# Performance work log

Measured on AMD Instinct MI355X. Metric: run time of the kernel, lower is better.

The kernel has to match this reference:

```python
import jax, jax.numpy as jnp
import numpy as np

D = 20       # bond_dim (= virtual_dim = per-module output_dim)
BATCH = 128
BN_EPS = 1e-5


def _unfold(t, h, w, n):
    # torch x.unfold(2,h,h).unfold(3,w,w).reshape(b, C, -1, n)
    B, C, H, W = t.shape
    t = t.reshape(B, C, H // h, h, W // w, w).transpose(0, 1, 2, 4, 3, 5)
    return t.reshape(B, C, -1, n)


def _mps(x, cores, label):
    # x: [b, C, P, n] site values; cores: [P, n, D, F, D] with F = 2*C; label: [P, D, O, D]
    feat = jnp.concatenate([x, 1.0 - x], axis=1)              # [b, F, P, n]  ([x, 1-x] feature map)
    M = jnp.einsum('bfpn,pnufv->npbuv', feat, cores)           # [n, P, b, D, D] site matrices
    v = jnp.full((cores.shape[2],), cores.shape[2] ** -0.5, dtype=x.dtype)  # boundary vector
    left = jnp.einsum('u,pbuv->pbv', v, M[0])
    for i in range(1, M.shape[0]):                             # n is small & static (4 or 16)
        left = jnp.einsum('pbu,pbuv->pbv', left, M[i])
    return jnp.einsum('pbu,puov,v->bpo', left, label, v)       # [b, P, O]


def _bn(y, gamma, beta):
    # training-mode BatchNorm1d over channel axis 1 of [b, C, L]
    mean = y.mean(axis=(0, 2), keepdims=True)
    var = y.var(axis=(0, 2), keepdims=True)
    return (y - mean) * jax.lax.rsqrt(var + BN_EPS) * gamma[None, :, None] + beta[None, :, None]


def setup_inputs() -> dict:
    key = jax.random.key(0)
    ks = jax.random.split(key, 9)
    f32 = jnp.float32
    def core(k, shape):
        F = shape[-2]
        return (jax.random.normal(k, shape, f32) * np.float32(np.sqrt(3.0 / (D * F))))
    def lab(k, shape):
        return jax.random.normal(k, shape, f32) * np.float32(D ** -0.5)
    x = jax.random.uniform(ks[0], (BATCH, 48, 32, 32), f32)
    return {
        'x': x,
        'cores1': core(ks[1], (256, 4, D, 96, D)), 'label1': lab(ks[2], (256, D, D, D)),
        'g1': jnp.ones(256, f32), 'b1': jnp.zeros(256, f32),
        'cores2': core(ks[3], (64, 4, D, 2 * D, D)), 'label2': lab(ks[4], (64, D, D, D)),
        'g2': jnp.ones(64, f32), 'b2': jnp.zeros(64, f32),
        'cores3': core(ks[5], (16, 4, D, 2 * D, D)), 'label3': lab(ks[6], (16, D, D, D)),
        'g3': jnp.ones(16, f32), 'b3': jnp.zeros(16, f32),
        'coresF': core(ks[7], (16, D, 2 * D, D)), 'labelF': lab(ks[8], (D, 10, D)),
    }


def reference(x, cores1, label1, g1, b1, cores2, label2, g2, b2,
              cores3, label3, g3, b3, coresF, labelF):
    b = x.shape[0]
    # stage 1: 256 patch-experts over 4 sites each
    x1 = _unfold(x, 16, 16, 4)                  # [b, 48, 256, 4]
    y = _mps(x1, cores1, label1)                # [b, 256, D]
    y = _bn(y, g1, b1).reshape(b, D, 16, 16)    # faithful patch<->bond mixing view
    # stage 2: 64 experts
    y2 = _unfold(y, 8, 8, 4)                    # [b, D, 64, 4]
    y = _mps(y2, cores2, label2)                # [b, 64, D]
    y = _bn(y, g2, b2).reshape(b, D, 8, 8)
    # stage 3: 16 experts
    y3 = _unfold(y, 4, 4, 4)                    # [b, D, 16, 4]
    y = _mps(y3, cores3, label3)                # [b, 16, D]
    y = _bn(y, g3, b3)
    # final MPS over the 16 expert outputs (channels = D)
    y = y.transpose(0, 2, 1)[:, :, None, :]     # [b, D, 1, 16]
    out = _mps(y, coresF[None], labelF[None])   # [b, 1, 10]
    return out[:, 0, :]                         # squeeze -> [b, 10]
```

## Files before the change

### kernel.cpp

```cpp
#include <hip/hip_runtime.h>

#define VB 0.22360679774997896f

typedef __attribute__((ext_vector_type(8))) _Float16 half8;
typedef __attribute__((ext_vector_type(4))) float f32x4;

#define Z1_OFF   0
#define Z2_OFF   655360
#define Z3_OFF   819200
#define GS1_OFF  860160
#define GQ1_OFF  860416
#define GS2_OFF  860672
#define GQ2_OFF  860736
#define GS3_OFF  860800
#define GQ3_OFF  860816
#define LV1_OFF  860832
#define LV2_OFF  963232
#define LV3_OFF  988832
#define XT_OFF   995232
#define WH2_OFF  7286688
#define WH3_OFF  10563488

#define WAVEBAR() __builtin_amdgcn_wave_barrier()

__global__ __launch_bounds__(256, 8)
void prep_kernel(const float* __restrict__ x,
                 const float* __restrict__ c2, const float* __restrict__ c3,
                 const float* __restrict__ l1, const float* __restrict__ l2,
                 const float* __restrict__ l3,
                 float* __restrict__ xT,
                 _Float16* __restrict__ Wh2, _Float16* __restrict__ Wh3,
                 float* __restrict__ v1, float* __restrict__ v2,
                 float* __restrict__ v3,
                 float* __restrict__ gzero)
{
    __shared__ __align__(16) float tS[16 * 193];
    const int tid = threadIdx.x;
    const int b   = blockIdx.x;

    if (b < 2048) {
        const int pix0 = (b & 63) * 16;
        const int bc0  = (b >> 6) * 192;
        #pragma unroll
        for (int k = 0; k < 3; ++k) {
            int i = tid + k * 256;
            int r = i >> 2, q = i & 3;
            float4 v = *(const float4*)(x + (size_t)(bc0 + r) * 1024 + pix0 + q * 4);
            tS[(q * 4 + 0) * 193 + r] = v.x;
            tS[(q * 4 + 1) * 193 + r] = v.y;
            tS[(q * 4 + 2) * 193 + r] = v.z;
            tS[(q * 4 + 3) * 193 + r] = v.w;
        }
        __syncthreads();
        #pragma unroll
        for (int k = 0; k < 3; ++k) {
            int o = tid + k * 256;
            int pp = o / 48, c4 = o - pp * 48;
            float4 v;
            v.x = tS[pp * 193 + c4 * 4 + 0];
            v.y = tS[pp * 193 + c4 * 4 + 1];
            v.z = tS[pp * 193 + c4 * 4 + 2];
            v.w = tS[pp * 193 + c4 * 4 + 3];
            *(float4*)(xT + (size_t)(pix0 + pp) * 6144 + bc0 + c4 * 4) = v;
        }
    } else if (b < 6048) {
        int gidx = (b - 2048) * 256 + tid;
        int bb = gidx / 640;
        int o  = gidx - bb * 640;
        const float* src;
        _Float16* dst;
        if (bb < 1280) { src = c2 + (size_t)bb * 3200;          dst = Wh2 + (size_t)bb * 5120; }
        else           { src = c3 + (size_t)(bb - 1280) * 3200; dst = Wh3 + (size_t)(bb - 1280) * 5120; }
        int q  = o >> 6, l = o & 63;
        int ks = q / 5, nt = q - ks * 5;
        int c  = nt * 16 + (l & 15);
        int ul = c / 20;
        int v  = c - ul * 20;
        int f0 = ks * 32 + ((l >> 4) << 3);
        half8 hv;
        if (f0 < 40) {
            const float* sp = src + ul * 800 + f0 * 20 + v;
            #pragma unroll
            for (int j = 0; j < 8; ++j) hv[j] = (_Float16)sp[j * 20];
        } else {
            #pragma unroll
            for (int j = 0; j < 8; ++j) hv[j] = (_Float16)0.f;
        }
        *(half8*)(dst + (size_t)o * 8) = hv;
    } else if (b < 6384) {
        const int bb = b - 6048;
        const float* lb;
        float* ov;
        if (bb < 256)      { lb = l1 + (size_t)bb * 8000;         ov = v1 + bb * 400; }
        else if (bb < 320) { lb = l2 + (size_t)(bb - 256) * 8000; ov = v2 + (bb - 256) * 400; }
        else               { lb = l3 + (size_t)(bb - 320) * 8000; ov = v3 + (bb - 320) * 400; }
        for (int i = tid; i < 400; i += 256) {
            const float4* s = (const float4*)(lb + i * 20);
            float acc = 0.f;
            #pragma unroll
            for (int t = 0; t < 5; ++t) {
                float4 w = s[t];
                acc += w.x + w.y + w.z + w.w;
            }
            ov[i] = acc * VB;
        }
    } else {
        for (int i = tid; i < 672; i += 256) gzero[i] = 0.f;
    }
}

#define CHUNKX(ucv, LAST)                                                     \
    {                                                                         \
        if (!(LAST)) {                                                        \
            _Pragma("unroll")                                                 \
            for (int k = 0; k < 8; ++k) {                                     \
                int i4 = tid + k * 256;                                       \
                if (i4 < 1920) wr[k] = *(const float4*)(wnext + i4 * 4);      \
            }                                                                 \
            wnext += 7680;                                                    \
        }                                                                     \
        f32x4 acc[5];                                                         \
        _Pragma("unroll")                                                     \
        for (int nt = 0; nt < 5; ++nt) acc[nt] = (f32x4){0.f, 0.f, 0.f, 0.f};\
        _Pragma("unroll")                                                     \
        for (int ks = 0; ks < 3; ++ks) {                                      \
            _Pragma("unroll")                                                 \
            for (int nt = 0; nt < 5; ++nt) {                                  \
                half8 bf = *(const half8*)&Fcur[((ks * 5 + nt) * 64 + l) * 8];\
                acc[nt] = __builtin_amdgcn_mfma_f32_16x16x32_f16(             \
                    af[ks], bf, acc[nt], 0, 0, 0);                            \
            }                                                                 \
        }                                                                     \
        _Pragma("unroll")                                                     \
        for (int nt = 0; nt < 5; ++nt) {                                      \
            _Pragma("unroll")                                                 \
            for (int r = 0; r < 4; ++r)                                       \
                Mw[(hi * 4 + r) * 84 + nt * 16 + row16] = acc[nt][r];         \
        }                                                                     \
        WAVEBAR();                                                            \
        _Pragma("unroll")                                                     \
        for (int ul = 0; ul < 4; ++ul) {                                      \
            float lvx = lw[bQ * 20 + (ucv) * 4 + ul];                         \
            _Pragma("unroll")                                                 \
            for (int j = 0; j < 5; ++j)                                       \
                lacc[j] += lvx * Mw[bQ * 84 + ul * 20 + mh * 5 + j];          \
        }                                                                     \
        WAVEBAR();                                                            \
        __syncthreads();                                                      \
        if (!(LAST)) {                                                        \
            _Pragma("unroll")                                                 \
            for (int k = 0; k < 8; ++k) {                                     \
                int i4 = tid + k * 256;                                       \
                if (i4 < 1920) {                                              \
                    float vals[4] = {wr[k].x, wr[k].y, wr[k].z, wr[k].w};     \
                    _Pragma("unroll")                                         \
                    for (int t = 0; t < 4; ++t)                               \
                        Fnxt[sAddr[k][t]] = (_Float16)vals[t];                \
                }                                                             \
            }                                                                 \
        }                                                                     \
        __syncthreads();                                                      \
        { _Float16* t_ = Fcur; Fcur = Fnxt; Fnxt = t_; }                      \
    }

__global__ __launch_bounds__(256, 2)
void fused1_kernel(const float* __restrict__ xT, const float* __restrict__ cores1,
                   const float* __restrict__ labv,
                   float* __restrict__ z1, float* __restrict__ gs, float* __restrict__ gq)
{
    __shared__ __align__(16) float xS[4 * 768];
    __shared__ __align__(16) _Float16 Fbuf[2][7680];
    __shared__ __align__(16) float MchunkS[4 * 16 * 84];
    __shared__ __align__(16) float leftS[4 * 320];

    const int tid = threadIdx.x;
    const int p   = blockIdx.x;
    const int bh  = blockIdx.y;
    const int wv  = tid >> 6, l = tid & 63;
    float* xSw = xS + wv * 768;
    float* Mw  = MchunkS + wv * 1344;
    float* lw  = leftS + wv * 320;
    const int row16 = l & 15, hi = l >> 4;
    const int bQ = l >> 2,   mh = l & 3;
    const int hh  = (p >> 7) * 16 + ((p >> 2) & 15);
    const int ww0 = ((p >> 6) & 1) * 16 + (p & 3) * 4;

    int sAddr[8][4];
    #pragma unroll
    for (int k = 0; k < 8; ++k) {
        int i4 = tid + k * 256;
        if (i4 < 1920) {
            #pragma unroll
            for (int t = 0; t < 4; ++t) {
                int e = i4 * 4 + t;
                int v = e % 20;
                int r = e / 20;
                int f = r % 96;
                int ul = r / 96;
                int c = ul * 20 + v;
                sAddr[k][t] = (((f >> 5) * 5 + (c >> 4)) * 64 +
                               ((f >> 3) & 3) * 16 + (c & 15)) * 8 + (f & 7);
            }
        }
    }

    #pragma unroll
    for (int j = 0; j < 5; ++j) lw[bQ * 20 + mh * 5 + j] = VB;
    WAVEBAR();

    float lacc[5] = {0.f, 0.f, 0.f, 0.f, 0.f};
    float4 wr[8];
    const float* wnext = cores1 + (size_t)p * 153600;

    #pragma unroll
    for (int k = 0; k < 8; ++k) {
        int i4 = tid + k * 256;
        if (i4 < 1920) wr[k] = *(const float4*)(wnext + i4 * 4);
    }
    wnext += 7680;
    _Float16* Fcur = &Fbuf[0][0];
    _Float16* Fnxt = &Fbuf[1][0];
    #pragma unroll
    for (int k = 0; k < 8; ++k) {
        int i4 = tid + k * 256;
        if (i4 < 1920) {
            float vals[4] = {wr[k].x, wr[k].y, wr[k].z, wr[k].w};
            #pragma unroll
            for (int t = 0; t < 4; ++t)
                Fcur[sAddr[k][t]] = (_Float16)vals[t];
        }
    }
    __syncthreads();

    #pragma unroll 1
    for (int n = 0; n < 4; ++n) {
        const float* xsl = xT + (size_t)(hh * 32 + ww0 + n) * 6144 + bh * 3072 + wv * 768;
        #pragma unroll
        for (int k = 0; k < 3; ++k) {
            float4 v = *(const float4*)(xsl + (l + k * 64) * 4);
            *(float4*)&xSw[(l + k * 64) * 4] = v;
        }
        WAVEBAR();
        half8 af[3];
        #pragma unroll
        for (int ks = 0; ks < 3; ++ks) {
            int f0 = ks * 32 + hi * 8;
            int cc = (f0 < 48) ? f0 : f0 - 48;
            float4 a  = *(const float4*)&xSw[row16 * 48 + cc];
            float4 b2 = *(const float4*)&xSw[row16 * 48 + cc + 4];
            float vv[8] = {a.x, a.y, a.z, a.w, b2.x, b2.y, b2.z, b2.w};
            bool inv = (f0 >= 48);
            half8 hv;
            #pragma unroll
            for (int j = 0; j < 8; ++j) hv[j] = (_Float16)(inv ? (1.f - vv[j]) : vv[j]);
            af[ks] = hv;
        }
        WAVEBAR();

        const bool last = (n == 3);
        CHUNKX(0, 0)
        CHUNKX(1, 0)
        CHUNKX(2, 0)
        CHUNKX(3, 0)
        CHUNKX(4, last)

        #pragma unroll
        for (int j = 0; j < 5; ++j) { lw[bQ * 20 + mh * 5 + j] = lacc[j]; lacc[j] = 0.f; }
        WAVEBAR();
    }

    const float* lvp = labv + p * 400;
    #pragma unroll
    for (int k = 0; k < 7; ++k) { int i = l + k * 64; if (i < 400) Mw[i] = lvp[i]; }
    WAVEBAR();
    float yv[5] = {0.f, 0.f, 0.f, 0.f, 0.f};
    #pragma unroll
    for (int u = 0; u < 20; ++u) {
        float lu = lw[bQ * 20 + u];
        #pragma unroll
        for (int j = 0; j < 5; ++j) yv[j] += lu * Mw[u * 20 + mh * 5 + j];
    }
    float s = 0.f, s2 = 0.f;
    #pragma unroll
    for (int j = 0; j < 5; ++j) {
        z1[(size_t)(bh * 64 + wv * 16 + bQ) * 5120 + p * 20 + mh * 5 + j] = yv[j];
        s += yv[j]; s2 += yv[j] * yv[j];
    }
    #pragma unroll
    for (int off = 32; off > 0; off >>= 1) {
        s  += __shfl_down(s, off);
        s2 += __shfl_down(s2, off);
    }
    if (l == 0) { atomicAdd(&gs[p], s); atomicAdd(&gq[p], s2); }
}

#define UCBODYN(ucv, CUR, NXT)                                                   \
    {                                                                            \
        if ((ucv) < 4) {                                                         \
            const _Float16* bptr = whp + (size_t)((ucv) + 1) * 5120;             \
            _Pragma("unroll")                                                    \
            for (int q = 0; q < 10; ++q)                                         \
                NXT[q] = *(const half8*)(bptr + (q * 64 + l) * 8);               \
        }                                                                        \
        f32x4 acc[5];                                                            \
        _Pragma("unroll")                                                        \
        for (int nt = 0; nt < 5; ++nt) acc[nt] = (f32x4){0.f, 0.f, 0.f, 0.f};    \
        _Pragma("unroll")                                                        \
        for (int ks = 0; ks < 2; ++ks) {                                         \
            _Pragma("unroll")                                                    \
            for (int nt = 0; nt < 5; ++nt)                                       \
                acc[nt] = __builtin_amdgcn_mfma_f32_16x16x32_f16(                \
                    af[ks], CUR[ks * 5 + nt], acc[nt], 0, 0, 0);                 \
        }                                                                        \
        _Pragma("unroll")                                                        \
        for (int nt = 0; nt < 5; ++nt) {                                         \
            _Pragma("unroll")                                                    \
            for (int r = 0; r < 4; ++r)                                          \
                Mw[(hi * 4 + r) * 84 + nt * 16 + row16] = acc[nt][r];            \
        }                                                                        \
        WAVEBAR();                                                               \
        _Pragma("unroll")                                                        \
        for (int ul = 0; ul < 4; ++ul) {                                         \
            float lvx = lw[bQ * 20 + (ucv) * 4 + ul];                            \
            _Pragma("unroll")                                                    \
            for (int j = 0; j < 5; ++j)                                          \
                lacc[j] += lvx * Mw[bQ * 84 + ul * 20 + mh * 5 + j];             \
        }                                                                        \
        WAVEBAR();                                                               \
    }

template <int STAGE>
__global__ __launch_bounds__(256, 2)
void fusedN_kernel(const float* __restrict__ zin, const _Float16* __restrict__ Wh,
                   const float* __restrict__ labv,
                   const float* __restrict__ gsin, const float* __restrict__ gqin,
                   const float* __restrict__ gam,  const float* __restrict__ bet,
                   float* __restrict__ zout,
                   float* __restrict__ gsout, float* __restrict__ gqout)
{
    constexpr int ZIN  = (STAGE == 2) ? 5120 : 1280;
    constexpr int ZOUT = (STAGE == 2) ? 1280 : 320;
    constexpr int JUMP = (STAGE == 2) ? 256 : 64;

    __shared__ __align__(16) float zS[4 * 320];
    __shared__ float scS[4 * 20], shS[4 * 20];
    __shared__ __align__(16) float MchunkS[4 * 16 * 84];
    __shared__ __align__(16) float leftS[4 * 320];

    const int tid = threadIdx.x;
    const int p   = blockIdx.x;
    const int bh  = blockIdx.y;
    const int wv  = tid >> 6, l = tid & 63;
    float* zSw = zS + wv * 320;
    float* scw = scS + wv * 20;
    float* shw = shS + wv * 20;
    float* Mw  = MchunkS + wv * 1344;
    float* lw  = leftS + wv * 320;
    const int row16 = l & 15, hi = l >> 4;
    const int bQ = l >> 2,   mh = l & 3;
    const int bg = bh * 64;

    #pragma unroll
    for (int j = 0; j < 5; ++j) lw[bQ * 20 + mh * 5 + j] = VB;
    WAVEBAR();

    float lacc[5] = {0.f, 0.f, 0.f, 0.f, 0.f};

    #pragma unroll 1
    for (int n = 0; n < 4; ++n) {
        int hh, ww;
        if (STAGE == 2) { hh = (p >> 5) * 8 + ((p >> 1) & 7); ww = ((p >> 4) & 1) * 8 + (p & 1) * 4 + n; }
        else            { hh = (p >> 3) * 4 + (p & 3);        ww = ((p >> 2) & 1) * 4 + n; }
        const int oo = (STAGE == 2) ? (hh * 16 + ww) : (hh * 8 + ww);

        if (l < 20) {
            int ch = (l * JUMP + oo) / 20;
            float mean = gsin[ch] * (1.f / 2560.f);
            float var  = gqin[ch] * (1.f / 2560.f) - mean * mean;
            float rstd = rsqrtf(var + 1e-5f);
            float sc = gam[ch] * rstd;
            scw[l] = sc;
            shw[l] = bet[ch] - mean * sc;
        }
        WAVEBAR();
        #pragma unroll
        for (int q = 0; q < 5; ++q) {
            int d = hi * 5 + q;
            float zraw = zin[(size_t)(bg + wv * 16 + row16) * ZIN + d * JUMP + oo];
            zSw[row16 * 20 + d] = zraw * scw[d] + shw[d];
        }
        WAVEBAR();
        half8 af[2];
        #pragma unroll
        for (int ks = 0; ks < 2; ++ks) {
            int f0 = ks * 32 + hi * 8;
            half8 hv;
            #pragma unroll
            for (int j = 0; j < 8; ++j) {
                int f = f0 + j;
                float val;
                if (f < 20)      val = zSw[row16 * 20 + f];
                else if (f < 40) val = 1.f - zSw[row16 * 20 + f - 20];
                else             val = 0.f;
                hv[j] = (_Float16)val;
            }
            af[ks] = hv;
        }
        WAVEBAR();

        const _Float16* whp = Wh + (size_t)((p * 4 + n) * 5) * 5120;
        half8 bA[10], bB[10];
        {
            #pragma unroll
            for (int q = 0; q < 10; ++q) bA[q] = *(const half8*)(whp + (q * 64 + l) * 8);
        }
        UCBODYN(0, bA, bB)
        UCBODYN(1, bB, bA)
        UCBODYN(2, bA, bB)
        UCBODYN(3, bB, bA)
        UCBODYN(4, bA, bB)

        #pragma unroll
        for (int j = 0; j < 5; ++j) { lw[bQ * 20 + mh * 5 + j] = lacc[j]; lacc[j] = 0.f; }
        WAVEBAR();
    }

    const float* lvp = labv + p * 400;
    #pragma unroll
    for (int k = 0; k < 7; ++k) { int i = l + k * 64; if (i < 400) Mw[i] = lvp[i]; }
    WAVEBAR();
    float yv[5] = {0.f, 0.f, 0.f, 0.f, 0.f};
    #pragma unroll
    for (int u = 0; u < 20; ++u) {
        float lu = lw[bQ * 20 + u];
        #pragma unroll
        for (int j = 0; j < 5; ++j) yv[j] += lu * Mw[u * 20 + mh * 5 + j];
    }
    float s = 0.f, s2 = 0.f;
    #pragma unroll
    for (int j = 0; j < 5; ++j) {
        zout[(size_t)(bg + wv * 16 + bQ) * ZOUT + p * 20 + mh * 5 + j] = yv[j];
        s += yv[j]; s2 += yv[j] * yv[j];
    }
    #pragma unroll
    for (int off = 32; off > 0; off >>= 1) {
        s  += __shfl_down(s, off);
        s2 += __shfl_down(s2, off);
    }
    if (l == 0) { atomicAdd(&gsout[p], s); atomicAdd(&gqout[p], s2); }
}

__global__ __launch_bounds__(256, 4)
void final_kernel(const float* __restrict__ z3,
                  const float* __restrict__ coresF,
                  const float* __restrict__ labelF,
                  const float* __restrict__ g3,
                  const float* __restrict__ b3,
                  const float* __restrict__ gsum3,
                  const float* __restrict__ gsq3,
                  float* __restrict__ out)
{
    __shared__ __align__(16) float fS[16 * 40];
    __shared__ __align__(16) float MS[16 * 400];
    __shared__ float lvS[200];
    __shared__ float scS[16], shS[16];
    __shared__ float leftS[20];

    const int b   = blockIdx.x;
    const int tid = threadIdx.x;

    if (tid < 16) {
        float mean = gsum3[tid] * (1.f / 2560.f);
        float var  = gsq3[tid] * (1.f / 2560.f) - mean * mean;
        float rstd = rsqrtf(var + 1e-5f);
        float sc   = g3[tid] * rstd;
        scS[tid] = sc;
        shS[tid] = b3[tid] - mean * sc;
    }
    __syncthreads();

    for (int i = tid; i < 640; i += 256) {
        int n = i / 40, f = i - n * 40;
        float raw = z3[(size_t)b * 320 + n * 20 + (f % 20)];
        float val = raw * scS[n] + shS[n];
        fS[i] = (f < 20) ? val : (1.f - val);
    }
    for (int i = tid; i < 200; i += 256) {
        int u = i / 10, o = i - u * 10;
        const float* lb = labelF + (size_t)(u * 10 + o) * 20;
        float s = 0.f;
        #pragma unroll
        for (int vv = 0; vv < 20; ++vv) s += lb[vv];
        lvS[i] = s * VB;
    }
    __syncthreads();

    for (int i = tid; i < 6400; i += 256) {
        int n = i / 400, uv = i - n * 400;
        int u = uv / 20, v = uv - u * 20;
        const float* wb = coresF + ((size_t)(n * 20 + u) * 40) * 20 + v;
        const float* fb = fS + n * 40;
        float acc = 0.f;
        #pragma unroll
        for (int f = 0; f < 40; ++f) acc += fb[f] * wb[f * 20];
        MS[i] = acc;
    }
    __syncthreads();

    if (tid < 64) {
        if (tid < 20) leftS[tid] = VB;
        WAVEBAR();
        #pragma unroll 1
        for (int n = 0; n < 16; ++n) {
            float tmp = 0.f;
            if (tid < 20) {
                #pragma unroll
                for (int u = 0; u < 20; ++u) tmp += leftS[u] * MS[n * 400 + u * 20 + tid];
            }
            WAVEBAR();
            if (tid < 20) leftS[tid] = tmp;
            WAVEBAR();
        }
        if (tid < 10) {
            float s = 0.f;
            #pragma unroll
            for (int u = 0; u < 20; ++u) s += leftS[u] * lvS[u * 10 + tid];
            out[b * 10 + tid] = s;
        }
    }
}

extern "C" void kernel_launch(void* const* d_in, const int* in_sizes, int n_in,
                              void* d_out, int out_size, void* d_ws, size_t ws_size,
                              hipStream_t stream)
{
    const float* x      = (const float*)d_in[0];
    const float* cores1 = (const float*)d_in[1];
    const float* label1 = (const float*)d_in[2];
    const float* g1     = (const float*)d_in[3];
    const float* b1     = (const float*)d_in[4];
    const float* cores2 = (const float*)d_in[5];
    const float* label2 = (const float*)d_in[6];
    const float* g2     = (const float*)d_in[7];
    const float* b2     = (const float*)d_in[8];
    const float* cores3 = (const float*)d_in[9];
    const float* label3 = (const float*)d_in[10];
    const float* g3     = (const float*)d_in[11];
    const float* b3     = (const float*)d_in[12];
    const float* coresF = (const float*)d_in[13];
    const float* labelF = (const float*)d_in[14];

    float* ws  = (float*)d_ws;
    float* z1  = ws + Z1_OFF;
    float* z2  = ws + Z2_OFF;
    float* z3  = ws + Z3_OFF;
    float* gs1 = ws + GS1_OFF; float* gq1 = ws + GQ1_OFF;
    float* gs2 = ws + GS2_OFF; float* gq2 = ws + GQ2_OFF;
    float* gs3 = ws + GS3_OFF; float* gq3 = ws + GQ3_OFF;
    float* lv1 = ws + LV1_OFF;
    float* lv2 = ws + LV2_OFF;
    float* lv3 = ws + LV3_OFF;
    float* xT  = ws + XT_OFF;
    _Float16* Wh2 = (_Float16*)(ws + WH2_OFF);
    _Float16* Wh3 = (_Float16*)(ws + WH3_OFF);

    prep_kernel<<<6385, 256, 0, stream>>>(x, cores2, cores3,
                                          label1, label2, label3,
                                          xT, Wh2, Wh3,
                                          lv1, lv2, lv3, gs1);

    fused1_kernel<<<dim3(256, 2), 256, 0, stream>>>(xT, cores1, lv1, z1, gs1, gq1);
    fusedN_kernel<2><<<dim3(64, 2), 256, 0, stream>>>(z1, Wh2, lv2, gs1, gq1, g1, b1,
                                                      z2, gs2, gq2);
    fusedN_kernel<3><<<dim3(16, 2), 256, 0, stream>>>(z2, Wh3, lv3, gs2, gq2, g2, b2,
                                                      z3, gs3, gq3);
    final_kernel<<<128, 256, 0, stream>>>(z3, coresF, labelF, g3, b3,
                                          gs3, gq3, (float*)d_out);
}
```

Measured before the change: 123.7 us.

## Drop input transpose pass and fuse whole batch per expert block in stage one

Removes the xT transpose stage from the prep kernel and has the stage-one kernel read x directly into registers, picking out each site's component from float4 loads. Stage one now uses one 512-thread block per patch covering the full batch instead of two 256-thread blocks, so each core slice is loaded and converted to fp16 once per patch rather than twice. Per-patch BN statistics are reduced in shared memory and written directly, replacing atomics. In exchange there are fewer blocks, larger LDS use per block, and strided global reads of x.

```diff
diff --git a/kernel.cpp b/kernel.cpp
--- a/kernel.cpp
+++ b/kernel.cpp
@@ -17,54 +17,25 @@
 #define LV1_OFF  860832
 #define LV2_OFF  963232
 #define LV3_OFF  988832
-#define XT_OFF   995232
-#define WH2_OFF  7286688
-#define WH3_OFF  10563488
+#define WH2_OFF  995232
+#define WH3_OFF  4272032
 
 #define WAVEBAR() __builtin_amdgcn_wave_barrier()
 
 __global__ __launch_bounds__(256, 8)
-void prep_kernel(const float* __restrict__ x,
-                 const float* __restrict__ c2, const float* __restrict__ c3,
+void prep_kernel(const float* __restrict__ c2, const float* __restrict__ c3,
                  const float* __restrict__ l1, const float* __restrict__ l2,
                  const float* __restrict__ l3,
-                 float* __restrict__ xT,
                  _Float16* __restrict__ Wh2, _Float16* __restrict__ Wh3,
                  float* __restrict__ v1, float* __restrict__ v2,
                  float* __restrict__ v3,
                  float* __restrict__ gzero)
 {
-    __shared__ __align__(16) float tS[16 * 193];
     const int tid = threadIdx.x;
     const int b   = blockIdx.x;
 
-    if (b < 2048) {
-        const int pix0 = (b & 63) * 16;
-        const int bc0  = (b >> 6) * 192;
-        #pragma unroll
-        for (int k = 0; k < 3; ++k) {
-            int i = tid + k * 256;
-            int r = i >> 2, q = i & 3;
-            float4 v = *(const float4*)(x + (size_t)(bc0 + r) * 1024 + pix0 + q * 4);
-            tS[(q * 4 + 0) * 193 + r] = v.x;
-            tS[(q * 4 + 1) * 193 + r] = v.y;
-            tS[(q * 4 + 2) * 193 + r] = v.z;
-            tS[(q * 4 + 3) * 193 + r] = v.w;
-        }
-        __syncthreads();
-        #pragma unroll
-        for (int k = 0; k < 3; ++k) {
-            int o = tid + k * 256;
-            int pp = o / 48, c4 = o - pp * 48;
-            float4 v;
-            v.x = tS[pp * 193 + c4 * 4 + 0];
-            v.y = tS[pp * 193 + c4 * 4 + 1];
-            v.z = tS[pp * 193 + c4 * 4 + 2];
-            v.w = tS[pp * 193 + c4 * 4 + 3];
-            *(float4*)(xT + (size_t)(pix0 + pp) * 6144 + bc0 + c4 * 4) = v;
-        }
-    } else if (b < 6048) {
-        int gidx = (b - 2048) * 256 + tid;
+    if (b < 4000) {
+        int gidx = b * 256 + tid;
         int bb = gidx / 640;
         int o  = gidx - bb * 640;
         const float* src;
@@ -87,8 +58,8 @@
             for (int j = 0; j < 8; ++j) hv[j] = (_Float16)0.f;
         }
         *(half8*)(dst + (size_t)o * 8) = hv;
-    } else if (b < 6384) {
-        const int bb = b - 6048;
+    } else if (b < 4336) {
+        const int bb = b - 4000;
         const float* lb;
         float* ov;
         if (bb < 256)      { lb = l1 + (size_t)bb * 8000;         ov = v1 + bb * 400; }
@@ -113,8 +84,8 @@
     {                                                                         \
         if (!(LAST)) {                                                        \
             _Pragma("unroll")                                                 \
-            for (int k = 0; k < 8; ++k) {                                     \
-                int i4 = tid + k * 256;                                       \
+            for (int k = 0; k < 4; ++k) {                                     \
+                int i4 = tid + k * 512;                                       \
                 if (i4 < 1920) wr[k] = *(const float4*)(wnext + i4 * 4);      \
             }                                                                 \
             wnext += 7680;                                                    \
@@ -149,8 +120,8 @@
         __syncthreads();                                                      \
         if (!(LAST)) {                                                        \
             _Pragma("unroll")                                                 \
-            for (int k = 0; k < 8; ++k) {                                     \
-                int i4 = tid + k * 256;                                       \
+            for (int k = 0; k < 4; ++k) {                                     \
+                int i4 = tid + k * 512;                                       \
                 if (i4 < 1920) {                                              \
                     float vals[4] = {wr[k].x, wr[k].y, wr[k].z, wr[k].w};     \
                     _Pragma("unroll")                                         \
@@ -163,19 +134,20 @@
         { _Float16* t_ = Fcur; Fcur = Fnxt; Fnxt = t_; }                      \
     }
 
-__global__ __launch_bounds__(256, 2)
-void fused1_kernel(const float* __restrict__ xT, const float* __restrict__ cores1,
+__global__ __launch_bounds__(512, 2)
+void fused1_kernel(const float* __restrict__ x, const float* __restrict__ cores1,
                    const float* __restrict__ labv,
                    float* __restrict__ z1, float* __restrict__ gs, float* __restrict__ gq)
 {
-    __shared__ __align__(16) float xS[4 * 768];
+    __shared__ __align__(16) float xS[8 * 768];
     __shared__ __align__(16) _Float16 Fbuf[2][7680];
-    __shared__ __align__(16) float MchunkS[4 * 16 * 84];
-    __shared__ __align__(16) float leftS[4 * 320];
+    __shared__ __align__(16) float MchunkS[8 * 16 * 84];
+    __shared__ __align__(16) float leftS[8 * 320];
+    __shared__ float redS[16];
 
     const int tid = threadIdx.x;
-    const int p   = blockIdx.x;
-    const int bh  = blockIdx.y;
+    const int bid = blockIdx.x;
+    const int p   = (bid & 7) * 32 + (bid >> 3);
     const int wv  = tid >> 6, l = tid & 63;
     float* xSw = xS + wv * 768;
     float* Mw  = MchunkS + wv * 1344;
@@ -185,10 +157,19 @@
     const int hh  = (p >> 7) * 16 + ((p >> 2) & 15);
     const int ww0 = ((p >> 6) & 1) * 16 + (p & 3) * 4;
 
-    int sAddr[8][4];
-    #pragma unroll
-    for (int k = 0; k < 8; ++k) {
-        int i4 = tid + k * 256;
+    float4 xr[12];
+    #pragma unroll
+    for (int k = 0; k < 12; ++k) {
+        int idx = l + k * 64;
+        int br = idx / 48, c = idx - br * 48;
+        xr[k] = *(const float4*)(x + (((size_t)((wv * 16 + br) * 48 + c)) << 10)
+                                   + hh * 32 + ww0);
+    }
+
+    int sAddr[4][4];
+    #pragma unroll
+    for (int k = 0; k < 4; ++k) {
+        int i4 = tid + k * 512;
         if (i4 < 1920) {
             #pragma unroll
             for (int t = 0; t < 4; ++t) {
@@ -209,20 +190,20 @@
     WAVEBAR();
 
     float lacc[5] = {0.f, 0.f, 0.f, 0.f, 0.f};
-    float4 wr[8];
+    float4 wr[4];
     const float* wnext = cores1 + (size_t)p * 153600;
 
     #pragma unroll
-    for (int k = 0; k < 8; ++k) {
-        int i4 = tid + k * 256;
+    for (int k = 0; k < 4; ++k) {
+        int i4 = tid + k * 512;
         if (i4 < 1920) wr[k] = *(const float4*)(wnext + i4 * 4);
     }
     wnext += 7680;
     _Float16* Fcur = &Fbuf[0][0];
     _Float16* Fnxt = &Fbuf[1][0];
     #pragma unroll
-    for (int k = 0; k < 8; ++k) {
-        int i4 = tid + k * 256;
+    for (int k = 0; k < 4; ++k) {
+        int i4 = tid + k * 512;
         if (i4 < 1920) {
             float vals[4] = {wr[k].x, wr[k].y, wr[k].z, wr[k].w};
             #pragma unroll
@@ -234,11 +215,12 @@
 
     #pragma unroll 1
     for (int n = 0; n < 4; ++n) {
-        const float* xsl = xT + (size_t)(hh * 32 + ww0 + n) * 6144 + bh * 3072 + wv * 768;
-        #pragma unroll
-        for (int k = 0; k < 3; ++k) {
-            float4 v = *(const float4*)(xsl + (l + k * 64) * 4);
-            *(float4*)&xSw[(l + k * 64) * 4] = v;
+        #pragma unroll
+        for (int k = 0; k < 12; ++k) {
+            int idx = l + k * 64;
+            float v = (n == 0) ? xr[k].x : (n == 1) ? xr[k].y
+                    : (n == 2) ? xr[k].z : xr[k].w;
+            xSw[idx] = v;
         }
         WAVEBAR();
         half8 af[3];
@@ -283,7 +265,7 @@
     float s = 0.f, s2 = 0.f;
     #pragma unroll
     for (int j = 0; j < 5; ++j) {
-        z1[(size_t)(bh * 64 + wv * 16 + bQ) * 5120 + p * 20 + mh * 5 + j] = yv[j];
+        z1[(size_t)(wv * 16 + bQ) * 5120 + p * 20 + mh * 5 + j] = yv[j];
         s += yv[j]; s2 += yv[j] * yv[j];
     }
     #pragma unroll
@@ -291,7 +273,14 @@
         s  += __shfl_down(s, off);
         s2 += __shfl_down(s2, off);
     }
-    if (l == 0) { atomicAdd(&gs[p], s); atomicAdd(&gq[p], s2); }
+    if (l == 0) { redS[wv] = s; redS[8 + wv] = s2; }
+    __syncthreads();
+    if (tid == 0) {
+        float S = 0.f, Q = 0.f;
+        #pragma unroll
+        for (int w2 = 0; w2 < 8; ++w2) { S += redS[w2]; Q += redS[8 + w2]; }
+        gs[p] = S; gq[p] = Q;
+    }
 }
 
 #define UCBODYN(ucv, CUR, NXT)                                                   \
@@ -560,16 +549,15 @@
     float* lv1 = ws + LV1_OFF;
     float* lv2 = ws + LV2_OFF;
     float* lv3 = ws + LV3_OFF;
-    float* xT  = ws + XT_OFF;
     _Float16* Wh2 = (_Float16*)(ws + WH2_OFF);
     _Float16* Wh3 = (_Float16*)(ws + WH3_OFF);
 
-    prep_kernel<<<6385, 256, 0, stream>>>(x, cores2, cores3,
+    prep_kernel<<<4337, 256, 0, stream>>>(cores2, cores3,
                                           label1, label2, label3,
-                                          xT, Wh2, Wh3,
+                                          Wh2, Wh3,
                                           lv1, lv2, lv3, gs1);
 
-    fused1_kernel<<<dim3(256, 2), 256, 0, stream>>>(xT, cores1, lv1, z1, gs1, gq1);
+    fused1_kernel<<<256, 512, 0, stream>>>(x, cores1, lv1, z1, gs1, gq1);
     fusedN_kernel<2><<<dim3(64, 2), 256, 0, stream>>>(z1, Wh2, lv2, gs1, gq1, g1, b1,
                                                       z2, gs2, gq2);
     fusedN_kernel<3><<<dim3(16, 2), 256, 0, stream>>>(z2, Wh3, lv3, gs2, gq2, g2, b2,
```

Result: faster. 113.0 us (-8.7%).
